# Performance work log

Hardware: AMD Instinct MI355X
Metric: run time of the kernel (lower is better)

## Reference

```python
import jax, jax.numpy as jnp
import numpy as np

N_BASIS = 8
BASIS_MAX_R = 2.0
BASIS_SIGMA = 0.25


def _radial_basis(difference_mat):
    # difference_mat: [n, b, a, 3] -> gaussian radial basis [n, b, a, K]
    r = jnp.linalg.norm(difference_mat, axis=-1)  # [n, b, a]
    centers = jnp.linspace(0.0, BASIS_MAX_R, N_BASIS, dtype=difference_mat.dtype)
    return jnp.exp(-((r[..., None] - centers) ** 2) / (2.0 * BASIS_SIGMA ** 2))


def setup_inputs() -> dict:
    key = jax.random.key(0)
    k1, k2, k3, k4 = jax.random.split(key, 4)
    n, c, d, p = 2, 8, 8, 1024
    input = jax.random.normal(k1, (n, c, p), dtype=jnp.float32)
    difference_mat = jax.random.normal(k2, (n, p, p, 3), dtype=jnp.float32)
    relative_mask = jax.random.uniform(k3, (n, p, p), dtype=jnp.float32)
    W = jax.random.normal(k4, (d, c, N_BASIS), dtype=jnp.float32) * 0.1
    return {"input": input, "difference_mat": difference_mat,
            "relative_mask": relative_mask, "W": W}


def reference(input, difference_mat, relative_mask, W):
    # kernel(difference_mat): [d, c, n, b, a] pairwise channel-mixing tensor
    basis = _radial_basis(difference_mat)                      # [n, b, a, K]
    kernel = jnp.einsum('dck,nbak->dcnba', W, basis)           # [d, c, n, b, a]
    # masked einsum: 'nba,dcnba->dcnba'
    kernel = kernel * relative_mask[None, None]                # broadcast mask
    # contraction: 'nca,dcnba->ndb'
    output = jnp.einsum('nca,dcnba->ndb', input, kernel)       # [n, d, b]
    return output
```

## Files before the change

### kernel.cpp

```cpp
#include <hip/hip_runtime.h>

#define P 1024
#define C 8
#define D 8
#define K 8

__global__ __launch_bounds__(256, 2) void se3_conv_kernel(
    const float* __restrict__ input,
    const float* __restrict__ diff,
    const float* __restrict__ mask,
    const float* __restrict__ W,
    float* __restrict__ out)
{
    const int b    = blockIdx.x;
    const int n    = blockIdx.y;
    const int tid  = threadIdx.x;
    const int lane = tid & 63;
    const int wave = tid >> 6;

    const float* diff_row = diff + (((size_t)n * P + b) * P) * 3;
    const float* mask_row = mask + ((size_t)n * P + b) * P;
    const float* inp_n    = input + (size_t)n * C * P;

    float acc[K * C];
    #pragma unroll
    for (int i = 0; i < K * C; ++i) acc[i] = 0.0f;

    const float step = 2.0f / 7.0f;

    #pragma unroll
    for (int j = 0; j < 4; ++j) {
        const int a = tid + j * 256;
        const float x = diff_row[a * 3 + 0];
        const float y = diff_row[a * 3 + 1];
        const float z = diff_row[a * 3 + 2];
        const float m = mask_row[a];
        const float r = sqrtf(x * x + y * y + z * z);

        float basis[K];
        #pragma unroll
        for (int k = 0; k < K; ++k) {
            const float t = r - step * (float)k;
            basis[k] = __expf(-8.0f * t * t) * m;
        }

        float inp[C];
        #pragma unroll
        for (int c = 0; c < C; ++c) inp[c] = inp_n[c * P + a];

        #pragma unroll
        for (int k = 0; k < K; ++k)
            #pragma unroll
            for (int c = 0; c < C; ++c)
                acc[k * C + c] += basis[k] * inp[c];
    }

    #pragma unroll
    for (int s = 0; s < 6; ++s) {
        const int half = 32 >> s;
        const int bit  = (lane >> s) & 1;
        #pragma unroll
        for (int i = 0; i < half; ++i) {
            const float send = bit ? acc[i] : acc[i + half];
            const float recv = __shfl_xor(send, 1 << s, 64);
            const float keep = bit ? acc[i + half] : acc[i];
            acc[i] = keep + recv;
        }
    }

    __shared__ float red[4][64];
    __shared__ float ttot[64];

    const int j64 = (int)(__brev((unsigned)lane) >> 26);
    red[wave][j64] = acc[0];
    __syncthreads();

    if (tid < 64) {
        ttot[tid] = red[0][tid] + red[1][tid] + red[2][tid] + red[3][tid];
    }
    __syncthreads();

    if (tid < D) {
        const int d = tid;
        float o = 0.0f;
        #pragma unroll
        for (int i = 0; i < 64; ++i) {
            const int k = i >> 3;
            const int c = i & 7;
            o += W[(d * C + c) * K + k] * ttot[i];
        }
        out[((size_t)n * D + d) * P + b] = o;
    }
}

extern "C" void kernel_launch(void* const* d_in, const int* in_sizes, int n_in,
                              void* d_out, int out_size, void* d_ws, size_t ws_size,
                              hipStream_t stream) {
    const float* input = (const float*)d_in[0];
    const float* diff  = (const float*)d_in[1];
    const float* mask  = (const float*)d_in[2];
    const float* W     = (const float*)d_in[3];
    float* out = (float*)d_out;

    dim3 grid(P, 2);
    se3_conv_kernel<<<grid, 256, 0, stream>>>(input, diff, mask, W, out);
}
```

Baseline: 17.92 us.

## Assign one wave per output row and stage input in LDS

Each block now handles four b rows, one per wave, and first copies the whole per-batch input tile (32 KB) into shared memory so all four waves reuse it. The Gaussian basis is rewritten as exp2 of a fused quadratic in r, and the final W contraction is spread across the wave using shuffles, which removes one block barrier. The cost is a 32 KB LDS footprint and a per-block input copy, which may limit occupancy. Each wave also now runs a 16-iteration loop instead of 4.

After: 19.40 us. 8.2% more time.

```diff
diff --git a/kernel.cpp b/kernel.cpp
--- a/kernel.cpp
+++ b/kernel.cpp
@@ -4,6 +4,8 @@
 #define C 8
 #define D 8
 #define K 8
+#define WPB 4
+#define AITER (P / 64)
 
 __global__ __launch_bounds__(256, 2) void se3_conv_kernel(
     const float* __restrict__ input,
@@ -12,47 +14,63 @@
     const float* __restrict__ W,
     float* __restrict__ out)
 {
-    const int b    = blockIdx.x;
+    __shared__ float inp_lds[C * P];
+    __shared__ float Tl[WPB][64];
+
     const int n    = blockIdx.y;
     const int tid  = threadIdx.x;
     const int lane = tid & 63;
     const int wave = tid >> 6;
+    const int b    = blockIdx.x * WPB + wave;
+
+    {
+        const float4* src = (const float4*)(input + (size_t)n * C * P);
+        float4* dst = (float4*)inp_lds;
+        #pragma unroll
+        for (int i = 0; i < (C * P / 4) / 256; ++i)
+            dst[tid + i * 256] = src[tid + i * 256];
+    }
+    __syncthreads();
 
     const float* diff_row = diff + (((size_t)n * P + b) * P) * 3;
     const float* mask_row = mask + ((size_t)n * P + b) * P;
-    const float* inp_n    = input + (size_t)n * C * P;
 
     float acc[K * C];
     #pragma unroll
     for (int i = 0; i < K * C; ++i) acc[i] = 0.0f;
 
-    const float step = 2.0f / 7.0f;
+    const float L2E = 1.44269504f;
 
-    #pragma unroll
-    for (int j = 0; j < 4; ++j) {
-        const int a = tid + j * 256;
+    #pragma unroll 4
+    for (int j = 0; j < AITER; ++j) {
+        const int a = lane + j * 64;
         const float x = diff_row[a * 3 + 0];
         const float y = diff_row[a * 3 + 1];
         const float z = diff_row[a * 3 + 2];
         const float m = mask_row[a];
-        const float r = sqrtf(x * x + y * y + z * z);
+
+        const float r2 = fmaf(x, x, fmaf(y, y, z * z));
+        const float r  = sqrtf(r2);
+        const float u  = -8.0f * L2E * r2;
 
         float basis[K];
         #pragma unroll
         for (int k = 0; k < K; ++k) {
-            const float t = r - step * (float)k;
-            basis[k] = __expf(-8.0f * t * t) * m;
+            const float ck = (2.0f / 7.0f) * (float)k;
+            const float c1 = 16.0f * L2E * ck;
+            const float c0 = -8.0f * L2E * ck * ck;
+            basis[k] = exp2f(fmaf(c1, r, c0) + u) * m;
         }
 
         float inp[C];
         #pragma unroll
-        for (int c = 0; c < C; ++c) inp[c] = inp_n[c * P + a];
+        for (int c = 0; c < C; ++c) inp[c] = inp_lds[c * P + a];
 
         #pragma unroll
         for (int k = 0; k < K; ++k)
             #pragma unroll
             for (int c = 0; c < C; ++c)
-                acc[k * C + c] += basis[k] * inp[c];
+                acc[k * C + c] = fmaf(basis[k], inp[c], acc[k * C + c]);
     }
 
     #pragma unroll
@@ -68,29 +86,21 @@
         }
     }
 
-    __shared__ float red[4][64];
-    __shared__ float ttot[64];
-
     const int j64 = (int)(__brev((unsigned)lane) >> 26);
-    red[wave][j64] = acc[0];
+    Tl[wave][j64] = acc[0];
     __syncthreads();
 
-    if (tid < 64) {
-        ttot[tid] = red[0][tid] + red[1][tid] + red[2][tid] + red[3][tid];
-    }
-    __syncthreads();
-
-    if (tid < D) {
-        const int d = tid;
-        float o = 0.0f;
-        #pragma unroll
-        for (int i = 0; i < 64; ++i) {
-            const int k = i >> 3;
-            const int c = i & 7;
-            o += W[(d * C + c) * K + k] * ttot[i];
-        }
-        out[((size_t)n * D + d) * P + b] = o;
-    }
+    const int d  = lane >> 3;
+    const int k8 = lane & 7;
+    float part = 0.0f;
+    #pragma unroll
+    for (int m = 0; m < 8; ++m)
+        part += W[d * 64 + m * 8 + k8] * Tl[wave][k8 * 8 + m];
+    part += __shfl_xor(part, 1, 64);
+    part += __shfl_xor(part, 2, 64);
+    part += __shfl_xor(part, 4, 64);
+    if (k8 == 0)
+        out[((size_t)n * D + d) * P + b] = part;
 }
 
 extern "C" void kernel_launch(void* const* d_in, const int* in_sizes, int n_in,
@@ -102,6 +112,6 @@
     const float* W     = (const float*)d_in[3];
     float* out = (float*)d_out;
 
-    dim3 grid(P, 2);
+    dim3 grid(P / WPB, 2);
     se3_conv_kernel<<<grid, 256, 0, stream>>>(input, diff, mask, W, out);
 }
```
